# Optimization experiments

Measured on AMD Instinct MI355X. Metric: run time of the kernel, lower is better.

Reference implementation:

```python
import jax, jax.numpy as jnp
import numpy as np

B, HD, H, W = 2, 4, 128, 128
KSIZE = 7
K = KSIZE * KSIZE
NSP = 9          # 3x3 superpixel candidates per pixel (hardcoded in CUDA ext)
S = 64           # number of superpixels (stride-16 grid on 128x128)


def setup_inputs() -> dict:
    key = jax.random.key(0)
    k1, k2, k3 = jax.random.split(key, 3)
    attn = jax.random.normal(k1, (B, HD, H, W, K), dtype=jnp.float32)
    sims = jax.random.uniform(k2, (B, S, H, W), dtype=jnp.float32)
    sinds = jax.random.randint(k3, (B, H, W, NSP), 0, S, dtype=jnp.int32)
    return {"attn": attn, "sims": sims, "sinds": sinds}


def _neighbor_coords(n, ks):
    # NAT-style clamped window: start = clip(i - ks//2, 0, n-ks)
    start = jnp.clip(jnp.arange(n) - ks // 2, 0, n - ks)
    return start[:, None] + jnp.arange(ks)[None, :]  # (n, ks)


def reference(attn, sims, sinds):
    eps = 1e-10
    b, hd, h, w, kk = attn.shape
    ks = int(round(kk ** 0.5))
    nsp = sinds.shape[-1]

    # stable exp of logits
    c = jnp.max(attn, axis=-1, keepdims=True)
    a = jnp.exp(attn - c)                                   # (B,HD,H,W,K)

    hj = _neighbor_coords(h, ks)                            # (H,ks)
    wj = _neighbor_coords(w, ks)                            # (W,ks)

    # p[b,h,w,s,kh,kw] = sims[b, sinds[b,h,w,s], hj[h,kh], wj[w,kw]]
    b_idx = jnp.arange(b)[:, None, None, None, None, None]
    gid = sinds[:, :, :, :, None, None]                     # (B,H,W,9,1,1)
    hj_e = hj[None, :, None, None, :, None]                 # (1,H,1,1,ks,1)
    wj_e = wj[None, None, :, None, None, :]                 # (1,1,W,1,1,ks)
    p = sims[b_idx, gid, hj_e, wj_e]                        # (B,H,W,9,ks,ks)
    p = p.reshape(b, h, w, nsp, kk).transpose(0, 3, 1, 2, 4)  # (B,9,H,W,K)

    # reweight: P(L_j = s) * exp(qk), then normalize over neighbors j
    ao = a[:, :, None, :, :, :] * p[:, None, :, :, :, :]    # (B,HD,9,H,W,K)
    ao = ao / (eps + jnp.sum(ao, axis=-1, keepdims=True))

    # pi[b,h,w,s] = P(L_i = s) = sims[b, sinds[b,h,w,s], h, w]
    h_idx = jnp.arange(h)[None, :, None, None]
    w_idx = jnp.arange(w)[None, None, :, None]
    pi = sims[jnp.arange(b)[:, None, None, None], sinds, h_idx, w_idx]  # (B,H,W,9)
    pi = pi.transpose(0, 3, 1, 2)[:, None, :, :, :, None]   # (B,1,9,H,W,1)

    return jnp.sum(pi * ao, axis=2)                         # (B,HD,H,W,K)
```

## Files before the change

### kernel.cpp

```cpp
#include <hip/hip_runtime.h>
#include <math.h>

#define BN   2
#define HDN  4
#define HN   128
#define WN   128
#define KS   7
#define KK   49
#define NSPN 9
#define TPB  128
#define PROW 52
#define PBUF 832
#define STG  3136
#define WREG (STG + 2 * PBUF)

#define CFENCE() asm volatile("" ::: "memory")

__global__ __launch_bounds__(TPB, 2) void attn_rw8(
    const float* __restrict__ attn,
    const float* __restrict__ sims,
    const int*   __restrict__ sinds,
    float*       __restrict__ out)
{
    __shared__ __align__(16) float smem[2 * WREG];
    __shared__ int g_lds[2][16 * NSPN];

    const int t    = threadIdx.x;
    const int lane = t & 63;
    const int wv   = t >> 6;
    const int bx   = blockIdx.x;
    const int wseg = bx & 3;
    const int hh   = (bx >> 2) & 127;
    const int b    = bx >> 9;
    const int ww0  = wseg * 32 + wv * 16;

    const int pixL = lane >> 2;
    const int hd   = lane & 3;

    const float* simsB = sims + ((size_t)b << 20);
    int hs = hh - 3; hs = max(0, min(HN - KS, hs));
    const int dr = hh - hs;

    float* stg = smem + wv * WREG;
    float* pb  = stg + STG;
    int*   gl  = g_lds[wv];

    {
        const int* ssrc = sinds + ((b * HN + hh) * WN + ww0) * NSPN;
        if (lane < 36) {
            int4 s;
            __builtin_memcpy(&s, ssrc + lane * 4, 16);
            *(int4*)(gl + lane * 4) = s;
        }
    }
    CFENCE();

    const size_t hwk   = (size_t)HN * WN * KK;
    const size_t pbase = (size_t)(hh * WN + ww0) * KK;
    const float* aB    = attn + (size_t)b * HDN * hwk + pbase;

    float4 s00,s01,s02,s03, s10,s11,s12,s13, s20,s21,s22,s23, s30,s31,s32,s33;
#define LDP(c, v0, v1, v2, v3) { \
        const float* g_ = aB + (size_t)(c) * hwk; \
        v0 = *(const float4*)(g_ + lane * 4); \
        v1 = *(const float4*)(g_ + 256 + lane * 4); \
        v2 = *(const float4*)(g_ + 512 + lane * 4); \
        v3 = make_float4(0.f, 0.f, 0.f, 0.f); \
        if (lane < 4) v3 = *(const float4*)(g_ + 768 + lane * 4); }
    LDP(0, s00, s01, s02, s03)
    LDP(1, s10, s11, s12, s13)
    LDP(2, s20, s21, s22, s23)
    LDP(3, s30, s31, s32, s33)
#undef LDP

    const int  gki     = lane / KS;
    const int  gkj     = lane - gki * KS;
    const bool gact    = lane < KK;
    const int  laneoff = gact ? (gki * WN + gkj) : 0;

    float gr[16];
    auto gissue = [&](int sp) {
        int gv = 0;
        if (lane < 16) gv = gl[lane * NSPN + sp];
        #pragma unroll
        for (int i = 0; i < 16; ++i) {
            int g  = __builtin_amdgcn_readlane(gv, i);
            int ws = ww0 + i - 3; ws = max(0, min(WN - KS, ws));
            if (gact) gr[i] = simsB[((size_t)g << 14) + hs * WN + ws + laneoff];
        }
    };
    auto gstore = [&](int buf) {
        if (gact) {
            #pragma unroll
            for (int i = 0; i < 16; ++i)
                pb[buf * PBUF + i * PROW + lane] = gr[i];
        }
    };

    gissue(0);

#define STP(c, v0, v1, v2, v3) { \
        float* d_ = stg + (c) * 784; \
        *(float4*)(d_ + lane * 4) = v0; \
        *(float4*)(d_ + 256 + lane * 4) = v1; \
        *(float4*)(d_ + 512 + lane * 4) = v2; \
        if (lane < 4) *(float4*)(d_ + 768 + lane * 4) = v3; }
    STP(0, s00, s01, s02, s03)
    STP(1, s10, s11, s12, s13)
    STP(2, s20, s21, s22, s23)
    STP(3, s30, s31, s32, s33)
#undef STP
    CFENCE();

    const int ab = hd * 784 + pixL * KK;
    float a[KK];
    #pragma unroll
    for (int k = 0; k < KK; ++k) a[k] = stg[ab + k];

    {
        float m0 = a[0], m1 = a[1], m2 = a[2], m3 = a[3];
        #pragma unroll
        for (int k = 4; k < KK; k += 4) {
            m0 = fmaxf(m0, a[k]);
            if (k + 1 < KK) m1 = fmaxf(m1, a[k + 1]);
            if (k + 2 < KK) m2 = fmaxf(m2, a[k + 2]);
            if (k + 3 < KK) m3 = fmaxf(m3, a[k + 3]);
        }
        float m = fmaxf(fmaxf(m0, m1), fmaxf(m2, m3));
        #pragma unroll
        for (int k = 0; k < KK; ++k) a[k] = __expf(a[k] - m);
    }

    gstore(0);

    const int wabs  = ww0 + pixL;
    const int wsp   = max(0, min(WN - KS, wabs - 3));
    const int dc    = wabs - wsp;
    const int pioff = pixL * PROW + dr * KS + dc;

    float acc[KK];
    #pragma unroll
    for (int k = 0; k < KK; ++k) acc[k] = 0.0f;

    for (int sp = 0; sp < NSPN; ++sp) {
        const int buf = sp & 1;
        if (sp + 1 < NSPN) gissue(sp + 1);
        CFENCE();

        float p[KK];
        const float* prow = pb + buf * PBUF + pixL * PROW;
        #pragma unroll
        for (int k4 = 0; k4 < 12; ++k4) {
            float4 v = *(const float4*)(prow + k4 * 4);
            p[k4 * 4 + 0] = v.x; p[k4 * 4 + 1] = v.y;
            p[k4 * 4 + 2] = v.z; p[k4 * 4 + 3] = v.w;
        }
        p[48] = prow[48];

        float d0 = 0.f, d1 = 0.f, d2 = 0.f, d3 = 0.f;
        #pragma unroll
        for (int k = 0; k < 48; k += 4) {
            d0 = fmaf(a[k + 0], p[k + 0], d0);
            d1 = fmaf(a[k + 1], p[k + 1], d1);
            d2 = fmaf(a[k + 2], p[k + 2], d2);
            d3 = fmaf(a[k + 3], p[k + 3], d3);
        }
        d0 = fmaf(a[48], p[48], d0);
        float d = (d0 + d1) + (d2 + d3);

        float pi   = pb[buf * PBUF + pioff];
        float coef = pi * __builtin_amdgcn_rcpf(d + 1e-10f);

        #pragma unroll
        for (int k = 0; k < KK; ++k) acc[k] = fmaf(coef, p[k], acc[k]);

        if (sp + 1 < NSPN) gstore(buf ^ 1);
    }

    #pragma unroll
    for (int k = 0; k < KK; ++k) stg[ab + k] = a[k] * acc[k];
    CFENCE();

    float* oB = out + (size_t)b * HDN * hwk + pbase;
    #pragma unroll
    for (int c = 0; c < 4; ++c) {
        const float* s_ = stg + c * 784;
        float*       o_ = oB + (size_t)c * hwk;
        float4 z0 = *(const float4*)(s_ + lane * 4);
        float4 z1 = *(const float4*)(s_ + 256 + lane * 4);
        float4 z2 = *(const float4*)(s_ + 512 + lane * 4);
        *(float4*)(o_ + lane * 4) = z0;
        *(float4*)(o_ + 256 + lane * 4) = z1;
        *(float4*)(o_ + 512 + lane * 4) = z2;
        if (lane < 4) {
            float4 z3 = *(const float4*)(s_ + 768 + lane * 4);
            *(float4*)(o_ + 768 + lane * 4) = z3;
        }
    }
}

extern "C" void kernel_launch(void* const* d_in, const int* in_sizes, int n_in,
                              void* d_out, int out_size, void* d_ws, size_t ws_size,
                              hipStream_t stream) {
    const float* attn  = (const float*)d_in[0];
    const float* sims  = (const float*)d_in[1];
    const int*   sinds = (const int*)d_in[2];
    float*       outp  = (float*)d_out;

    const int blocks = BN * HN * (WN / 32);
    attn_rw8<<<blocks, TPB, 0, stream>>>(attn, sims, sinds, outp);
}
```

Baseline: 100.1 us.

## Gather sims window rows as float4 loads and alias P buffer onto staging LDS

Replaces the per-lane scalar gather (16 scalar loads per lane per superpixel, 49 active lanes) with 4 float4 loads per lane. Each load fetches half of a 7-wide window row: elements 0-3, or 3-6 stored as 4-7. The results go into a padded 8-wide row layout in LDS. The P double buffer now reuses the attn staging region instead of separate LDS space, which cuts shared memory per block. The change depends on the staging area being dead once the a[] values are in registers, and on the overlapping half-row loads being correct near edges.

```diff
diff --git a/kernel.cpp b/kernel.cpp
--- a/kernel.cpp
+++ b/kernel.cpp
@@ -9,20 +9,19 @@
 #define KK   49
 #define NSPN 9
 #define TPB  128
-#define PROW 52
-#define PBUF 832
+#define PIXSTR 60
+#define PBUF (16 * PIXSTR)
 #define STG  3136
-#define WREG (STG + 2 * PBUF)
 
 #define CFENCE() asm volatile("" ::: "memory")
 
-__global__ __launch_bounds__(TPB, 2) void attn_rw8(
+__global__ __launch_bounds__(TPB, 2) void attn_rw9(
     const float* __restrict__ attn,
     const float* __restrict__ sims,
     const int*   __restrict__ sinds,
     float*       __restrict__ out)
 {
-    __shared__ __align__(16) float smem[2 * WREG];
+    __shared__ __align__(16) float smem[2 * STG];
     __shared__ int g_lds[2][16 * NSPN];
 
     const int t    = threadIdx.x;
@@ -41,8 +40,8 @@
     int hs = hh - 3; hs = max(0, min(HN - KS, hs));
     const int dr = hh - hs;
 
-    float* stg = smem + wv * WREG;
-    float* pb  = stg + STG;
+    float* stg = smem + wv * STG;
+    float* pb  = stg;
     int*   gl  = g_lds[wv];
 
     {
@@ -73,27 +72,39 @@
     LDP(3, s30, s31, s32, s33)
 #undef LDP
 
-    const int  gki     = lane / KS;
-    const int  gkj     = lane - gki * KS;
-    const bool gact    = lane < KK;
-    const int  laneoff = gact ? (gki * WN + gkj) : 0;
-
-    float gr[16];
+    const int  grp   = min(lane / 14, 3);
+    const int  cp    = lane - grp * 14;
+    const int  grow  = min(cp >> 1, 6);
+    const int  ghalf = cp & 1;
+    const bool gact  = lane < 56;
+    int pixs[4], wss[4];
+    #pragma unroll
+    for (int i = 0; i < 4; ++i) {
+        pixs[i] = 4 * i + grp;
+        wss[i]  = max(0, min(WN - KS, ww0 + pixs[i] - 3));
+    }
+    const int rowoff = (hs + grow) * WN + ghalf * 3;
+
+    float4 q0, q1, q2, q3;
     auto gissue = [&](int sp) {
-        int gv = 0;
-        if (lane < 16) gv = gl[lane * NSPN + sp];
-        #pragma unroll
-        for (int i = 0; i < 16; ++i) {
-            int g  = __builtin_amdgcn_readlane(gv, i);
-            int ws = ww0 + i - 3; ws = max(0, min(WN - KS, ws));
-            if (gact) gr[i] = simsB[((size_t)g << 14) + hs * WN + ws + laneoff];
+        int g0 = gl[pixs[0] * NSPN + sp];
+        int g1 = gl[pixs[1] * NSPN + sp];
+        int g2 = gl[pixs[2] * NSPN + sp];
+        int g3 = gl[pixs[3] * NSPN + sp];
+        if (gact) {
+            __builtin_memcpy(&q0, simsB + ((size_t)g0 << 14) + rowoff + wss[0], 16);
+            __builtin_memcpy(&q1, simsB + ((size_t)g1 << 14) + rowoff + wss[1], 16);
+            __builtin_memcpy(&q2, simsB + ((size_t)g2 << 14) + rowoff + wss[2], 16);
+            __builtin_memcpy(&q3, simsB + ((size_t)g3 << 14) + rowoff + wss[3], 16);
         }
     };
     auto gstore = [&](int buf) {
+        float* d = pb + buf * PBUF;
         if (gact) {
-            #pragma unroll
-            for (int i = 0; i < 16; ++i)
-                pb[buf * PBUF + i * PROW + lane] = gr[i];
+            *(float4*)(d + pixs[0] * PIXSTR + grow * 8 + ghalf * 4) = q0;
+            *(float4*)(d + pixs[1] * PIXSTR + grow * 8 + ghalf * 4) = q1;
+            *(float4*)(d + pixs[2] * PIXSTR + grow * 8 + ghalf * 4) = q2;
+            *(float4*)(d + pixs[3] * PIXSTR + grow * 8 + ghalf * 4) = q3;
         }
     };
 
@@ -130,53 +141,59 @@
         #pragma unroll
         for (int k = 0; k < KK; ++k) a[k] = __expf(a[k] - m);
     }
+    CFENCE();
 
     gstore(0);
 
     const int wabs  = ww0 + pixL;
     const int wsp   = max(0, min(WN - KS, wabs - 3));
     const int dc    = wabs - wsp;
-    const int pioff = pixL * PROW + dr * KS + dc;
+    const int dcs   = dc + (dc > 3 ? 1 : 0);
+    const int pioff = pixL * PIXSTR + dr * 8 + dcs;
 
     float acc[KK];
     #pragma unroll
     for (int k = 0; k < KK; ++k) acc[k] = 0.0f;
+
+    #define P(k) p[(k) / KS][(k) % KS]
 
     for (int sp = 0; sp < NSPN; ++sp) {
         const int buf = sp & 1;
         if (sp + 1 < NSPN) gissue(sp + 1);
         CFENCE();
 
-        float p[KK];
-        const float* prow = pb + buf * PBUF + pixL * PROW;
-        #pragma unroll
-        for (int k4 = 0; k4 < 12; ++k4) {
-            float4 v = *(const float4*)(prow + k4 * 4);
-            p[k4 * 4 + 0] = v.x; p[k4 * 4 + 1] = v.y;
-            p[k4 * 4 + 2] = v.z; p[k4 * 4 + 3] = v.w;
-        }
-        p[48] = prow[48];
+        float p[KS][KS];
+        const float* prow = pb + buf * PBUF + pixL * PIXSTR;
+        #pragma unroll
+        for (int r = 0; r < KS; ++r) {
+            float4 lo = *(const float4*)(prow + r * 8);
+            float4 hi = *(const float4*)(prow + r * 8 + 4);
+            p[r][0] = lo.x; p[r][1] = lo.y; p[r][2] = lo.z; p[r][3] = lo.w;
+            p[r][4] = hi.y; p[r][5] = hi.z; p[r][6] = hi.w;
+        }
 
         float d0 = 0.f, d1 = 0.f, d2 = 0.f, d3 = 0.f;
         #pragma unroll
         for (int k = 0; k < 48; k += 4) {
-            d0 = fmaf(a[k + 0], p[k + 0], d0);
-            d1 = fmaf(a[k + 1], p[k + 1], d1);
-            d2 = fmaf(a[k + 2], p[k + 2], d2);
-            d3 = fmaf(a[k + 3], p[k + 3], d3);
-        }
-        d0 = fmaf(a[48], p[48], d0);
+            d0 = fmaf(a[k + 0], P(k + 0), d0);
+            d1 = fmaf(a[k + 1], P(k + 1), d1);
+            d2 = fmaf(a[k + 2], P(k + 2), d2);
+            d3 = fmaf(a[k + 3], P(k + 3), d3);
+        }
+        d0 = fmaf(a[48], P(48), d0);
         float d = (d0 + d1) + (d2 + d3);
 
         float pi   = pb[buf * PBUF + pioff];
         float coef = pi * __builtin_amdgcn_rcpf(d + 1e-10f);
 
         #pragma unroll
-        for (int k = 0; k < KK; ++k) acc[k] = fmaf(coef, p[k], acc[k]);
+        for (int k = 0; k < KK; ++k) acc[k] = fmaf(coef, P(k), acc[k]);
 
         if (sp + 1 < NSPN) gstore(buf ^ 1);
     }
-
+    #undef P
+
+    CFENCE();
     #pragma unroll
     for (int k = 0; k < KK; ++k) stg[ab + k] = a[k] * acc[k];
     CFENCE();
@@ -208,5 +225,5 @@
     float*       outp  = (float*)d_out;
 
     const int blocks = BN * HN * (WN / 32);
-    attn_rw8<<<blocks, TPB, 0, stream>>>(attn, sims, sinds, outp);
+    attn_rw9<<<blocks, TPB, 0, stream>>>(attn, sims, sinds, outp);
 }
```

Measured after the change: 95.49 us. -4.6%, faster.

## Gather sims via global_load_lds with triple-buffered pipeline and halved staging

Applied to the files above, without the earlier changes.

Replaces the per-lane scalar sims gather through registers with 16-byte global_load_lds transfers straight into LDS. The loads feed a three-deep buffer ring, and explicit vmcnt waits keep up to three superpixel gathers in flight. The attn staging area is halved by staging two head channels at a time, which cuts LDS use per wave. This aims to remove register round-trips and raise memory-level parallelism for the gather. In exchange it loads padded 8-wide rows, which wastes some bandwidth, and it depends on hand-counted vmcnt values being correct.

```diff
diff --git a/kernel.cpp b/kernel.cpp
--- a/kernel.cpp
+++ b/kernel.cpp
@@ -9,14 +9,20 @@
 #define KK   49
 #define NSPN 9
 #define TPB  128
-#define PROW 52
-#define PBUF 832
-#define STG  3136
-#define WREG (STG + 2 * PBUF)
+#define ISTR 260
+#define GBUF (4 * ISTR)
+#define NBUF 3
+#define STGD 1568
+#define WREG (STGD + NBUF * GBUF)
 
 #define CFENCE() asm volatile("" ::: "memory")
 
-__global__ __launch_bounds__(TPB, 2) void attn_rw8(
+#define GLDS(srcp, ldsp) \
+    __builtin_amdgcn_global_load_lds( \
+        (const __attribute__((address_space(1))) void*)(srcp), \
+        (__attribute__((address_space(3))) void*)(ldsp), 16, 0, 0)
+
+__global__ __launch_bounds__(TPB, 2) void attn_rw11(
     const float* __restrict__ attn,
     const float* __restrict__ sims,
     const int*   __restrict__ sinds,
@@ -42,18 +48,14 @@
     const int dr = hh - hs;
 
     float* stg = smem + wv * WREG;
-    float* pb  = stg + STG;
+    float* pbw = stg + STGD;
     int*   gl  = g_lds[wv];
 
+    int4 sreg = make_int4(0, 0, 0, 0);
     {
         const int* ssrc = sinds + ((b * HN + hh) * WN + ww0) * NSPN;
-        if (lane < 36) {
-            int4 s;
-            __builtin_memcpy(&s, ssrc + lane * 4, 16);
-            *(int4*)(gl + lane * 4) = s;
-        }
-    }
-    CFENCE();
+        if (lane < 36) __builtin_memcpy(&sreg, ssrc + lane * 4, 16);
+    }
 
     const size_t hwk   = (size_t)HN * WN * KK;
     const size_t pbase = (size_t)(hh * WN + ww0) * KK;
@@ -73,49 +75,61 @@
     LDP(3, s30, s31, s32, s33)
 #undef LDP
 
-    const int  gki     = lane / KS;
-    const int  gkj     = lane - gki * KS;
-    const bool gact    = lane < KK;
-    const int  laneoff = gact ? (gki * WN + gkj) : 0;
-
-    float gr[16];
-    auto gissue = [&](int sp) {
-        int gv = 0;
-        if (lane < 16) gv = gl[lane * NSPN + sp];
-        #pragma unroll
-        for (int i = 0; i < 16; ++i) {
-            int g  = __builtin_amdgcn_readlane(gv, i);
-            int ws = ww0 + i - 3; ws = max(0, min(WN - KS, ws));
-            if (gact) gr[i] = simsB[((size_t)g << 14) + hs * WN + ws + laneoff];
-        }
-    };
-    auto gstore = [&](int buf) {
-        if (gact) {
-            #pragma unroll
-            for (int i = 0; i < 16; ++i)
-                pb[buf * PBUF + i * PROW + lane] = gr[i];
-        }
-    };
-
-    gissue(0);
-
-#define STP(c, v0, v1, v2, v3) { \
-        float* d_ = stg + (c) * 784; \
+    if (lane < 36) *(int4*)(gl + lane * 4) = sreg;
+    CFENCE();
+
+    const int grp   = min(lane / 14, 3);
+    const int cp    = lane - grp * 14;
+    const int grow  = min(cp >> 1, 6);
+    const int ghalf = cp & 1;
+    const int pixs0 = grp,      pixs1 = 4 + grp;
+    const int pixs2 = 8 + grp,  pixs3 = 12 + grp;
+    const int wss0 = max(0, min(WN - KS, ww0 + pixs0 - 3));
+    const int wss1 = max(0, min(WN - KS, ww0 + pixs1 - 3));
+    const int wss2 = max(0, min(WN - KS, ww0 + pixs2 - 3));
+    const int wss3 = max(0, min(WN - KS, ww0 + pixs3 - 3));
+    const int rowoff = (hs + grow) * WN + ghalf * 3;
+
+#define ISSUE(sp, buf) { \
+        int g0_ = gl[pixs0 * NSPN + (sp)]; \
+        int g1_ = gl[pixs1 * NSPN + (sp)]; \
+        int g2_ = gl[pixs2 * NSPN + (sp)]; \
+        int g3_ = gl[pixs3 * NSPN + (sp)]; \
+        float* bb_ = pbw + (buf) * GBUF; \
+        GLDS(simsB + ((size_t)g0_ << 14) + rowoff + wss0, bb_); \
+        GLDS(simsB + ((size_t)g1_ << 14) + rowoff + wss1, bb_ + ISTR); \
+        GLDS(simsB + ((size_t)g2_ << 14) + rowoff + wss2, bb_ + 2 * ISTR); \
+        GLDS(simsB + ((size_t)g3_ << 14) + rowoff + wss3, bb_ + 3 * ISTR); }
+
+    ISSUE(0, 0)
+    ISSUE(1, 1)
+    ISSUE(2, 2)
+
+    float a[KK];
+#define STP(slot, v0, v1, v2, v3) { \
+        float* d_ = stg + (slot) * 784; \
         *(float4*)(d_ + lane * 4) = v0; \
         *(float4*)(d_ + 256 + lane * 4) = v1; \
         *(float4*)(d_ + 512 + lane * 4) = v2; \
         if (lane < 4) *(float4*)(d_ + 768 + lane * 4) = v3; }
     STP(0, s00, s01, s02, s03)
     STP(1, s10, s11, s12, s13)
-    STP(2, s20, s21, s22, s23)
-    STP(3, s30, s31, s32, s33)
+    CFENCE();
+    if (hd < 2) {
+        const int ab_ = hd * 784 + pixL * KK;
+        #pragma unroll
+        for (int k = 0; k < KK; ++k) a[k] = stg[ab_ + k];
+    }
+    CFENCE();
+    STP(0, s20, s21, s22, s23)
+    STP(1, s30, s31, s32, s33)
+    CFENCE();
+    if (hd >= 2) {
+        const int ab_ = (hd - 2) * 784 + pixL * KK;
+        #pragma unroll
+        for (int k = 0; k < KK; ++k) a[k] = stg[ab_ + k];
+    }
 #undef STP
-    CFENCE();
-
-    const int ab = hd * 784 + pixL * KK;
-    float a[KK];
-    #pragma unroll
-    for (int k = 0; k < KK; ++k) a[k] = stg[ab + k];
 
     {
         float m0 = a[0], m1 = a[1], m2 = a[2], m3 = a[3];
@@ -131,72 +145,83 @@
         for (int k = 0; k < KK; ++k) a[k] = __expf(a[k] - m);
     }
 
-    gstore(0);
-
-    const int wabs  = ww0 + pixL;
-    const int wsp   = max(0, min(WN - KS, wabs - 3));
-    const int dc    = wabs - wsp;
-    const int pioff = pixL * PROW + dr * KS + dc;
+    const int ipix    = pixL >> 2;
+    const int grpv    = pixL & 3;
+    const int pixbase = ipix * ISTR + grpv * 56;
+    const int wabs    = ww0 + pixL;
+    const int wsp     = max(0, min(WN - KS, wabs - 3));
+    const int dc      = wabs - wsp;
+    const int pidw    = dr * 8 + dc + (dc > 3 ? 1 : 0);
 
     float acc[KK];
     #pragma unroll
     for (int k = 0; k < KK; ++k) acc[k] = 0.0f;
 
-    for (int sp = 0; sp < NSPN; ++sp) {
-        const int buf = sp & 1;
-        if (sp + 1 < NSPN) gissue(sp + 1);
-        CFENCE();
-
-        float p[KK];
-        const float* prow = pb + buf * PBUF + pixL * PROW;
-        #pragma unroll
-        for (int k4 = 0; k4 < 12; ++k4) {
-            float4 v = *(const float4*)(prow + k4 * 4);
-            p[k4 * 4 + 0] = v.x; p[k4 * 4 + 1] = v.y;
-            p[k4 * 4 + 2] = v.z; p[k4 * 4 + 3] = v.w;
-        }
-        p[48] = prow[48];
-
-        float d0 = 0.f, d1 = 0.f, d2 = 0.f, d3 = 0.f;
-        #pragma unroll
-        for (int k = 0; k < 48; k += 4) {
-            d0 = fmaf(a[k + 0], p[k + 0], d0);
-            d1 = fmaf(a[k + 1], p[k + 1], d1);
-            d2 = fmaf(a[k + 2], p[k + 2], d2);
-            d3 = fmaf(a[k + 3], p[k + 3], d3);
-        }
-        d0 = fmaf(a[48], p[48], d0);
-        float d = (d0 + d1) + (d2 + d3);
-
-        float pi   = pb[buf * PBUF + pioff];
-        float coef = pi * __builtin_amdgcn_rcpf(d + 1e-10f);
-
-        #pragma unroll
-        for (int k = 0; k < KK; ++k) acc[k] = fmaf(coef, p[k], acc[k]);
-
-        if (sp + 1 < NSPN) gstore(buf ^ 1);
-    }
-
-    #pragma unroll
-    for (int k = 0; k < KK; ++k) stg[ab + k] = a[k] * acc[k];
-    CFENCE();
+#define P_(k) p[(k) / KS][(k) % KS]
+#define PHASE(sp, vmlit) { \
+        asm volatile("s_waitcnt vmcnt(" vmlit ")" ::: "memory"); \
+        const float* pp_ = pbw + ((sp) % NBUF) * GBUF + pixbase; \
+        float p[KS][KS]; \
+        _Pragma("unroll") \
+        for (int r = 0; r < KS; ++r) { \
+            float4 lo = *(const float4*)(pp_ + r * 8); \
+            float4 hi = *(const float4*)(pp_ + r * 8 + 4); \
+            p[r][0] = lo.x; p[r][1] = lo.y; p[r][2] = lo.z; p[r][3] = lo.w; \
+            p[r][4] = hi.y; p[r][5] = hi.z; p[r][6] = hi.w; } \
+        float pi_ = pp_[pidw]; \
+        CFENCE();                             \
+        if ((sp) + NBUF < NSPN) { ISSUE((sp) + NBUF, (sp) % NBUF) } \
+        float d0 = 0.f, d1 = 0.f, d2 = 0.f, d3 = 0.f; \
+        _Pragma("unroll") \
+        for (int k = 0; k < 48; k += 4) { \
+            d0 = fmaf(a[k + 0], P_(k + 0), d0); \
+            d1 = fmaf(a[k + 1], P_(k + 1), d1); \
+            d2 = fmaf(a[k + 2], P_(k + 2), d2); \
+            d3 = fmaf(a[k + 3], P_(k + 3), d3); } \
+        d0 = fmaf(a[48], P_(48), d0); \
+        float dd_ = (d0 + d1) + (d2 + d3); \
+        float coef_ = pi_ * __builtin_amdgcn_rcpf(dd_ + 1e-10f); \
+        _Pragma("unroll") \
+        for (int k = 0; k < KK; ++k) acc[k] = fmaf(coef_, P_(k), acc[k]); }
+
+    PHASE(0, "8") PHASE(1, "8") PHASE(2, "8")
+    PHASE(3, "8") PHASE(4, "8") PHASE(5, "8")
+    PHASE(6, "8") PHASE(7, "4") PHASE(8, "0")
+#undef PHASE
+#undef P_
+#undef ISSUE
 
     float* oB = out + (size_t)b * HDN * hwk + pbase;
-    #pragma unroll
-    for (int c = 0; c < 4; ++c) {
-        const float* s_ = stg + c * 784;
-        float*       o_ = oB + (size_t)c * hwk;
-        float4 z0 = *(const float4*)(s_ + lane * 4);
-        float4 z1 = *(const float4*)(s_ + 256 + lane * 4);
-        float4 z2 = *(const float4*)(s_ + 512 + lane * 4);
-        *(float4*)(o_ + lane * 4) = z0;
-        *(float4*)(o_ + 256 + lane * 4) = z1;
-        *(float4*)(o_ + 512 + lane * 4) = z2;
-        if (lane < 4) {
-            float4 z3 = *(const float4*)(s_ + 768 + lane * 4);
-            *(float4*)(o_ + 768 + lane * 4) = z3;
-        }
-    }
+#define OUTC(c, slot) { \
+        const float* s_ = stg + (slot) * 784; \
+        float*       o_ = oB + (size_t)(c) * hwk; \
+        float4 z0 = *(const float4*)(s_ + lane * 4); \
+        float4 z1 = *(const float4*)(s_ + 256 + lane * 4); \
+        float4 z2 = *(const float4*)(s_ + 512 + lane * 4); \
+        *(float4*)(o_ + lane * 4) = z0; \
+        *(float4*)(o_ + 256 + lane * 4) = z1; \
+        *(float4*)(o_ + 512 + lane * 4) = z2; \
+        if (lane < 4) { \
+            float4 z3 = *(const float4*)(s_ + 768 + lane * 4); \
+            *(float4*)(o_ + 768 + lane * 4) = z3; } }
+
+    CFENCE();
+    if (hd < 2) {
+        const int ab_ = hd * 784 + pixL * KK;
+        #pragma unroll
+        for (int k = 0; k < KK; ++k) stg[ab_ + k] = a[k] * acc[k];
+    }
+    CFENCE();
+    OUTC(0, 0) OUTC(1, 1)
+    CFENCE();
+    if (hd >= 2) {
+        const int ab_ = (hd - 2) * 784 + pixL * KK;
+        #pragma unroll
+        for (int k = 0; k < KK; ++k) stg[ab_ + k] = a[k] * acc[k];
+    }
+    CFENCE();
+    OUTC(2, 0) OUTC(3, 1)
+#undef OUTC
 }
 
 extern "C" void kernel_launch(void* const* d_in, const int* in_sizes, int n_in,
@@ -208,5 +233,5 @@
     float*       outp  = (float*)d_out;
 
     const int blocks = BN * HN * (WN / 32);
-    attn_rw8<<<blocks, TPB, 0, stream>>>(attn, sims, sinds, outp);
+    attn_rw11<<<blocks, TPB, 0, stream>>>(attn, sims, sinds, outp);
 }
```

After: 98.72 us. About the same (-1.4%).
